# Kernel tuning notes

Hardware: AMD Instinct MI355X
Metric: run time of the kernel (lower is better)

The kernel has to match this reference:

```python
import jax, jax.numpy as jnp
import numpy as np

N, D, E = 100000, 128, 1600000
C = 1.0
MIN_NORM = 1e-15   # hgcn min_norm clamp
BALL_EPS = 4e-3    # float32 eps for proj onto Poincare ball


def artanh(x):
    # hgcn Artanh clamps input away from +-1 (use 1e-7, the fp32-representable analog of 1e-15)
    return jnp.arctanh(jnp.clip(x, -1.0 + 1e-7, 1.0 - 1e-7))


def _norm(x):
    return jnp.maximum(jnp.linalg.norm(x, axis=-1, keepdims=True), MIN_NORM)


def proj(x, c):
    norm = _norm(x)
    maxnorm = (1.0 - BALL_EPS) / jnp.sqrt(c)
    return jnp.where(norm > maxnorm, x / norm * maxnorm, x)


def expmap0(u, c):
    sc = jnp.sqrt(c)
    n = _norm(u)
    return jnp.tanh(sc * n) * u / (sc * n)


def logmap0(p, c):
    sc = jnp.sqrt(c)
    n = _norm(p)
    return artanh(sc * n) * p / (sc * n)


def mobius_add(x, y, c):
    x2 = jnp.sum(x * x, -1, keepdims=True)
    y2 = jnp.sum(y * y, -1, keepdims=True)
    xy = jnp.sum(x * y, -1, keepdims=True)
    num = (1.0 + 2.0 * c * xy + c * y2) * x + (1.0 - c * x2) * y
    den = 1.0 + 2.0 * c * xy + c * c * x2 * y2
    return num / jnp.maximum(den, MIN_NORM)


def mobius_matvec(m, x, c):
    sc = jnp.sqrt(c)
    xn = _norm(x)
    mx = x @ m.T
    mxn = _norm(mx)
    res = jnp.tanh(mxn / xn * artanh(sc * xn)) * mx / (mxn * sc)
    zero = jnp.all(mx == 0, axis=-1, keepdims=True)
    return jnp.where(zero, jnp.zeros_like(res), res)


def hgc_layer(x, edge_index, edge_weight, w, b, c_in, c_out, n):
    # HypLinear: mobius matvec + hyperbolic bias
    h = proj(mobius_matvec(w, x, c_in), c_in)
    hyp_b = proj(expmap0(b[None, :], c_in), c_in)
    h = proj(mobius_add(h, hyp_b, c_in), c_in)
    # HypAgg: aggregate in tangent space via sparse adjacency (spmm)
    xt = logmap0(h, c_in)                                   # [N, D]
    msg = xt[edge_index[1]] * edge_weight[:, None]          # [E, D]
    agg = jax.ops.segment_sum(msg, edge_index[0], num_segments=n)
    h = proj(expmap0(agg, c_in), c_in)
    # HypAct: relu in tangent space, re-map to ball at c_out
    xt = jax.nn.relu(logmap0(h, c_in))
    return proj(expmap0(xt, c_out), c_out)


def setup_inputs() -> dict:
    key = jax.random.key(0)
    ks = jax.random.split(key, 8)
    x = jax.random.normal(ks[0], (N, D), dtype=jnp.float32)
    edge_index = jax.random.randint(ks[1], (2, E), 0, N, dtype=jnp.int64 if jax.config.jax_enable_x64 else jnp.int32)
    edge_weight = jax.random.uniform(ks[2], (E,), dtype=jnp.float32)
    s = 1.0 / np.sqrt(D)
    w1 = jax.random.normal(ks[3], (D, D), dtype=jnp.float32) * s
    b1 = jax.random.normal(ks[4], (D,), dtype=jnp.float32) * s
    w2 = jax.random.normal(ks[5], (D, D), dtype=jnp.float32) * s
    b2 = jax.random.normal(ks[6], (D,), dtype=jnp.float32) * s
    return {"x": x, "edge_index": edge_index, "edge_weight": edge_weight,
            "w1": w1, "b1": b1, "w2": w2, "b2": b2}


def reference(x, edge_index, edge_weight, w1, b1, w2, b2):
    c = jnp.float32(C)
    n = x.shape[0]
    # encode(): proj_tan0 is identity on the Poincare ball
    xh = proj(expmap0(x, c), c)
    h = hgc_layer(xh, edge_index, edge_weight, w1, b1, c, c, n)
    h = hgc_layer(h, edge_index, edge_weight, w2, b2, c, c, n)
    return h
```

## Files before the change

kernel.cpp:

```cpp
#include <hip/hip_runtime.h>
#include <math.h>
#include <stdint.h>

#define D 128
#define MAXNORM (1.0f - 4e-3f)
#define ART_CLAMP 0.9999999f
#define BKT_BITS 7
#define BKT_NODES 128
#define BKT_CAP 4096
#define NB_ROWN 1024

typedef __attribute__((ext_vector_type(8))) short short8;
typedef __attribute__((ext_vector_type(4))) float float4v;
typedef __attribute__((ext_vector_type(4))) int intv4;

__device__ __forceinline__ float waveAllReduce(float v) {
#pragma unroll
    for (int off = 32; off; off >>= 1) v += __shfl_xor(v, off, 64);
    return v;
}

__device__ __forceinline__ float reduce16(float v) {
    v += __shfl_xor(v, 8, 64);
    v += __shfl_xor(v, 4, 64);
// ... 197 lines not shown
    int wv = tid >> 6;
    int tx = lane & 15;
    int q = lane >> 4;
    int sw = tx & 7;
    int row0 = rowOff + gbid * 64;

    short8 wh[2][4], wl[2][4];
#pragma unroll
    for (int c = 0; c < 2; c++) {
        int wrow = 16 * (2 * wv + c) + tx;
        const uint16_t* ph = Whi + (size_t)wrow * D + q * 8;
        const uint16_t* pl = Wlo + (size_t)wrow * D + q * 8;
#pragma unroll
        for (int t = 0; t < 4; t++) {
            wh[c][t] = *(const short8*)(ph + t * 32);
            wl[c][t] = *(const short8*)(pl + t * 32);
        }
    }

    float hbf[8];
#pragma unroll
    for (int c = 0; c < 8; c++) hbf[c] = HB[16 * c + tx];
    float hbsq = 0.f;
#pragma unroll
    for (int c = 0; c < 8; c++) hbsq += hbf[c] * hbf[c];
    float hb2 = reduce16(hbsq);

    auto loadA = [&](int tau, float4& v0, float4& v1) {
        int gr = row0 + tau * 16 + tx;
        if (gr >= n) gr = n - 1;
        const float4* ap = (const float4*)(A + (size_t)gr * D + wv * 32 + q * 8);
        v0 = ap[0];
        v1 = ap[1];
    };
    auto splitStore = [&](int b, float4 v0, float4 v1) {
        float v[8] = {v0.x, v0.y, v0.z, v0.w, v1.x, v1.y, v1.z, v1.w};
        short8 hi, lo;
        split8(v, &hi, &lo);
        int pch = (4 * wv + q) ^ sw;
        L->Ah[b][tx][pch] = hi;
        L->Al[b][tx][pch] = lo;
    };

    float4 pa0, pa1;
    loadA(0, pa0, pa1);
    splitStore(0, pa0, pa1);
    loadA(1, pa0, pa1);
    __syncthreads();

#pragma unroll
    for (int tau = 0; tau < 4; tau++) {
        int b = tau & 1;
        float4v acc[2];
        acc[0] = (float4v){0.f, 0.f, 0.f, 0.f};
        acc[1] = (float4v){0.f, 0.f, 0.f, 0.f};
#pragma unroll
        for (int t = 0; t < 4; t++) {
            int pch = (4 * t + q) ^ sw;
            short8 ahi = L->Ah[b][tx][pch];
            short8 alo = L->Al[b][tx][pch];
#pragma unroll
            for (int c = 0; c < 2; c++) {
                acc[c] = __builtin_amdgcn_mfma_f32_16x16x32_bf16(ahi, wh[c][t], acc[c], 0, 0, 0);
                acc[c] = __builtin_amdgcn_mfma_f32_16x16x32_bf16(ahi, wl[c][t], acc[c], 0, 0, 0);
                acc[c] = __builtin_amdgcn_mfma_f32_16x16x32_bf16(alo, wh[c][t], acc[c], 0, 0, 0);
            }
        }

#pragma unroll
        for (int c = 0; c < 2; c++) {
            int col = 16 * (2 * wv + c) + tx;
#pragma unroll
            for (int p = 0; p < 4; p++) {
                int lr = 4 * q + p;
                L->Cs[lr * CS_STRIDE + ((col + 4 * lr) & 127)] = acc[c][p];
            }
        }

        if (tau < 3) {
            splitStore(b ^ 1, pa0, pa1);
            if (tau < 2) loadA(tau + 2, pa0, pa1);
        }
        __syncthreads();

        int lr = 4 * wv + q;
        int row = row0 + tau * 16 + lr;
        if (row < n) {
            float y[8];
#pragma unroll
            for (int c = 0; c < 8; c++)
                y[c] = L->Cs[lr * CS_STRIDE + ((16 * c + tx + 4 * lr) & 127)];

            float s = 0.f;
#pragma unroll
            for (int c = 0; c < 8; c++) s += y[c] * y[c];
            float yn2 = reduce16(s);
            float sc, xns;
            if (ENCODE) {
                float nn = fmaxf(XN[row], 1e-15f);
                float t = fast_tanh(nn);
                sc = t * rcpf(nn);
                float pn = fmaxf(t, 1e-15f);
                if (pn > MAXNORM) { sc *= MAXNORM * rcpf(pn); pn = MAXNORM; }
                xns = pn;
            } else {
                sc = 1.0f;
                xns = fmaxf(XN[row], 1e-15f);
            }
            float mxn2 = sc * sc * yn2;
            float mxn = fmaxf(fsqrtf(mxn2), 1e-15f);
            float arg = (mxn * rcpf(xns)) * fast_atanh(fminf(xns, ART_CLAMP));
            float t = fast_tanh(arg);
            float s2 = (mxn2 == 0.0f) ? 0.0f : (sc * t * rcpf(mxn));
            float h[8];
#pragma unroll
            for (int c = 0; c < 8; c++) h[c] = y[c] * s2;
            float rn = fmaxf(t, 1e-15f);
            float hn = rn;
            if (rn > MAXNORM) {
                float f = MAXNORM * rcpf(rn);
#pragma unroll
                for (int c = 0; c < 8; c++) h[c] *= f;
                hn = MAXNORM;
            }
            float x2 = hn * hn;
            float d0 = 0.f;
#pragma unroll
            for (int c = 0; c < 8; c++) d0 += h[c] * hbf[c];
            float xy = reduce16(d0);
            float k1 = 1.0f + 2.0f * xy + hb2;
            float k2 = 1.0f - x2;
            float den = fmaxf(1.0f + 2.0f * xy + x2 * hb2, 1e-15f);
            float rden = rcpf(den);
            float av[8];
            float s3 = 0.f;
#pragma unroll
            for (int c = 0; c < 8; c++) {
                av[c] = (k1 * h[c] + k2 * hbf[c]) * rden;
                s3 += av[c] * av[c];
            }
            float an = fmaxf(fsqrtf(reduce16(s3)), 1e-15f);
            float fproj = 1.0f;
            if (an > MAXNORM) { fproj = MAXNORM * rcpf(an); an = MAXNORM; }
            float lm = fproj * fast_atanh(fminf(an, ART_CLAMP)) * rcpf(an);
            uint16_t* o = XT + (size_t)row * D + tx;
#pragma unroll
            for (int c = 0; c < 8; c++) o[16 * c] = f2bf(av[c] * lm);
        }
        __syncthreads();
    }
}


__global__ __launch_bounds__(256) void fusedPre(
    const float* __restrict__ X, float* __restrict__ XN, int n,
    const int* __restrict__ DST, int* __restrict__ bcnt, int* __restrict__ Hcnt,
    int E, int B, int gH,
    const float* __restrict__ W1, const float* __restrict__ W2,
    uint16_t* __restrict__ Whi1, uint16_t* __restrict__ Wlo1,
    uint16_t* __restrict__ Whi2, uint16_t* __restrict__ Wlo2,
    const float* __restrict__ B1, const float* __restrict__ B2,
    float* __restrict__ HBOUT) {
    __shared__ int cnt[1024];
    int bid = blockIdx.x, tid = threadIdx.x;
    if (bid < NB_ROWN) {
        rowNorms_body(bid, tid, X, XN, n);
    } else if (bid < NB_ROWN + gH) {
        histo_body(bid - NB_ROWN, tid, DST, bcnt, Hcnt, E, B, cnt);
    } else if (bid < NB_ROWN + gH + 64) {
        prepW_body(bid - NB_ROWN - gH, tid, W1, W2, Whi1, Wlo1, Whi2, Wlo2);
    } else {
        bias_body(bid - NB_ROWN - gH - 64, tid, B1, B2, HBOUT);
    }
}

__global__ __launch_bounds__(1024) void bucketScan(const int* __restrict__ bcnt,
                                                   int* __restrict__ boff,
                                                   int* __restrict__ rp_last,
                                                   int B, int E) {
    __shared__ int sd[1024];
    int tid = threadIdx.x;
    int v = (tid < B) ? bcnt[tid] : 0;
    sd[tid] = v;
    __syncthreads();
    for (int off = 1; off < 1024; off <<= 1) {
        int t = (tid >= off) ? sd[tid - off] : 0;
        __syncthreads();
        sd[tid] += t;
        __syncthreads();
    }
    int ex = sd[tid] - v;
    if (tid < B) boff[tid] = ex;
    if (tid == 0) { boff[B] = E; *rp_last = E; }
}

__global__ __launch_bounds__(256) void scanA(const int* __restrict__ boff,
                                             const int* __restrict__ Hcnt,
                                             int* __restrict__ Hbase, int B, int gH) {
    __shared__ int sd[256];
    int b = blockIdx.x;
    int k = threadIdx.x;
    int base0 = boff[b];
    int carry = 0;
    for (int k0 = 0; k0 < gH; k0 += 256) {
        int kk = k0 + k;
        int v = (kk < gH) ? Hcnt[(size_t)kk * B + b] : 0;
        sd[k] = v;
        __syncthreads();
        for (int off = 1; off < 256; off <<= 1) {
            int t = (k >= off) ? sd[k - off] : 0;
            __syncthreads();
            sd[k] += t;
            __syncthreads();
        }
        if (kk < gH) Hbase[(size_t)kk * B + b] = base0 + carry + sd[k] - v;
        carry += sd[255];
        __syncthreads();
    }
}

__global__ __launch_bounds__(256, 3) void fusedBinGemm(
    const int* __restrict__ DST, const int* __restrict__ SRC,
    const float* __restrict__ EW, const int* __restrict__ Hbase,
    int2* __restrict__ binned, int E, int B, int gBin,
    const float* __restrict__ A, const uint16_t* __restrict__ Whi,
    const uint16_t* __restrict__ Wlo, const float* __restrict__ XN,
    const float* __restrict__ HB, uint16_t* __restrict__ XT, int n) {
    __shared__ LdsBG u;
    int bid = blockIdx.x, tid = threadIdx.x;
    if (bid < gBin)
        binEdges_body(bid, tid, DST, SRC, EW, Hbase, binned, E, B, u.b.cnt, u.b.base);
    else
        gemm_body<true>(bid - gBin, 0, tid, A, Whi, Wlo, XN, HB, XT, n, &u.g);
}

__global__ __launch_bounds__(256, 3) void fusedSortGemm(
    int2* __restrict__ binned, const int* __restrict__ boff,
    int* __restrict__ rp, int n, int gSort,
    const float* __restrict__ A, const uint16_t* __restrict__ Whi,
    const uint16_t* __restrict__ Wlo, const float* __restrict__ XN,
    const float* __restrict__ HB, uint16_t* __restrict__ XT, int rowOff) {
    __shared__ LdsSG u;
    int bid = blockIdx.x, tid = threadIdx.x;
    if (bid < gSort)
        sort_body(bid, tid, binned, boff, rp, n, u.s.cnt, u.s.cur, u.s.buf);
    else
        gemm_body<true>(bid - gSort, rowOff, tid, A, Whi, Wlo, XN, HB, XT, n, &u.g);
}

template <bool ENCODE>
__global__ __launch_bounds__(256, 3) void gemmM(const float* __restrict__ A,
                                                const uint16_t* __restrict__ Whi,
                                                const uint16_t* __restrict__ Wlo,
                                                const float* __restrict__ XN,
                                                const float* __restrict__ HB,
                                                uint16_t* __restrict__ XT, int n) {
    __shared__ GemmLds L;
    gemm_body<ENCODE>(blockIdx.x, 0, threadIdx.x, A, Whi, Wlo, XN, HB, XT, n, &L);
}


template <bool STORE_HN>
__global__ __launch_bounds__(256) void aggC(const uint16_t* __restrict__ XT,
                                            const int* __restrict__ rp,
                                            const int2* __restrict__ sorted,
                                            float* __restrict__ OUT,
                                            float* __restrict__ HN, int n) {
    int tid = threadIdx.x;
    int lane = tid & 63;
    int q = lane >> 4;
    int tx = lane & 15;
    int wv = (blockIdx.x * 256 + tid) >> 6;
    int g = wv * 4 + q;
    bool valid = (g < n);
    int gc = valid ? g : (n - 1);
    uint32_t beg = (uint32_t)rp[gc];
    uint32_t end = valid ? (uint32_t)rp[gc + 1] : beg;
    uint32_t deg = end - beg;

    int m = (int)deg;
    m = max(m, __shfl_xor(m, 16, 64));
    m = max(m, __shfl_xor(m, 32, 64));
    int ms = __builtin_amdgcn_readfirstlane(m);

    const char* sbase = (const char*)sorted;
    const char* xbase = (const char*)XT;
    uint32_t txoff = (uint32_t)tx * 16u;
    uint32_t jb = beg * 8u;
    uint32_t jendb = end * 8u;
    uint32_t jlastb = (jendb > 0u) ? (jendb - 8u) : 0u;

    float a[8];
#pragma unroll
    for (int c = 0; c < 8; c++) a[c] = 0.f;

    int2 e0 = *(const int2*)(sbase + min(jb, jlastb));
    int2 e1 = *(const int2*)(sbase + min(jb + 8u, jlastb));
    int2 e2 = *(const int2*)(sbase + min(jb + 16u, jlastb));
    int2 e3 = *(const int2*)(sbase + min(jb + 24u, jlastb));
    for (int i = 0; i < ms; i += 4) {
        int2 f0 = *(const int2*)(sbase + min(jb + 32u, jlastb));
        int2 f1 = *(const int2*)(sbase + min(jb + 40u, jlastb));
        int2 f2 = *(const int2*)(sbase + min(jb + 48u, jlastb));
        int2 f3 = *(const int2*)(sbase + min(jb + 56u, jlastb));
        intv4 u0 = *(const intv4*)(xbase + ((((uint32_t)e0.x) << 8) + txoff));
        intv4 u1 = *(const intv4*)(xbase + ((((uint32_t)e1.x) << 8) + txoff));
        intv4 u2 = *(const intv4*)(xbase + ((((uint32_t)e2.x) << 8) + txoff));
        intv4 u3 = *(const intv4*)(xbase + ((((uint32_t)e3.x) << 8) + txoff));
        float w0 = (jb < jendb) ? __int_as_float(e0.y) : 0.f;
        float w1 = (jb + 8u < jendb) ? __int_as_float(e1.y) : 0.f;
        float w2 = (jb + 16u < jendb) ? __int_as_float(e2.y) : 0.f;
        float w3 = (jb + 24u < jendb) ? __int_as_float(e3.y) : 0.f;
#pragma unroll
        for (int k = 0; k < 4; k++) {
            a[2 * k]     = fmaf(__uint_as_float(((uint32_t)u0[k]) << 16), w0, a[2 * k]);
            a[2 * k + 1] = fmaf(__uint_as_float(((uint32_t)u0[k]) & 0xFFFF0000u), w0, a[2 * k + 1]);
        }
#pragma unroll
        for (int k = 0; k < 4; k++) {
            a[2 * k]     = fmaf(__uint_as_float(((uint32_t)u1[k]) << 16), w1, a[2 * k]);
            a[2 * k + 1] = fmaf(__uint_as_float(((uint32_t)u1[k]) & 0xFFFF0000u), w1, a[2 * k + 1]);
        }
#pragma unroll
        for (int k = 0; k < 4; k++) {
            a[2 * k]     = fmaf(__uint_as_float(((uint32_t)u2[k]) << 16), w2, a[2 * k]);
            a[2 * k + 1] = fmaf(__uint_as_float(((uint32_t)u2[k]) & 0xFFFF0000u), w2, a[2 * k + 1]);
        }
#pragma unroll
        for (int k = 0; k < 4; k++) {
            a[2 * k]     = fmaf(__uint_as_float(((uint32_t)u3[k]) << 16), w3, a[2 * k]);
            a[2 * k + 1] = fmaf(__uint_as_float(((uint32_t)u3[k]) & 0xFFFF0000u), w3, a[2 * k + 1]);
        }
        jb += 32u;
        e0 = f0; e1 = f1; e2 = f2; e3 = f3;
    }

    float ss = 0.f;
#pragma unroll
    for (int c = 0; c < 8; c++) ss += a[c] * a[c];
    float nn = fmaxf(fsqrtf(reduce16(ss)), 1e-15f);
    float t = fast_tanh(nn);
    float sc = t * rcpf(nn);
    float pn = fmaxf(t, 1e-15f);
    if (pn > MAXNORM) { sc *= MAXNORM * rcpf(pn); pn = MAXNORM; }
    float lm = fast_atanh(fminf(pn, ART_CLAMP)) * rcpf(pn);
    float r[8];
    float ss2 = 0.f;
#pragma unroll
    for (int c = 0; c < 8; c++) {
        r[c] = fmaxf(lm * sc * a[c], 0.f);
        ss2 += r[c] * r[c];
    }
    float rn = fmaxf(fsqrtf(reduce16(ss2)), 1e-15f);
    float t2 = fast_tanh(rn);
    float sc2 = t2 * rcpf(rn);
    float on = fmaxf(t2, 1e-15f);
    if (on > MAXNORM) { sc2 *= MAXNORM * rcpf(on); on = MAXNORM; }
    if (valid) {
        float4* o = (float4*)(OUT + (size_t)g * D + tx * 8);
        o[0] = make_float4(r[0] * sc2, r[1] * sc2, r[2] * sc2, r[3] * sc2);
        o[1] = make_float4(r[4] * sc2, r[5] * sc2, r[6] * sc2, r[7] * sc2);
        if (STORE_HN && tx == 0) HN[g] = on;
    }
}


extern "C" void kernel_launch(void* const* d_in, const int* in_sizes, int n_in,
                              void* d_out, int out_size, void* d_ws, size_t ws_size,
                              hipStream_t stream) {
    const float* x  = (const float*)d_in[0];
    const int*   ei = (const int*)d_in[1];
    const float* ew = (const float*)d_in[2];
    const float* w1 = (const float*)d_in[3];
    const float* b1 = (const float*)d_in[4];
    const float* w2 = (const float*)d_in[5];
    const float* b2 = (const float*)d_in[6];
    int n = in_sizes[0] / D;
    int E = in_sizes[2];
    int B = (n + BKT_NODES - 1) >> BKT_BITS;

    uint16_t* xtb = (uint16_t*)d_ws;
    int*   bcnt = (int*)(xtb + (size_t)n * D);
    int*   boff = bcnt + 1024;
    int*   gcur = boff + 1025;
    int*   rp   = gcur + 1024;
    float* xn   = (float*)(rp + n + 1);
    uint16_t* whi1 = (uint16_t*)(((uintptr_t)(xn + n) + 15) & ~(uintptr_t)15);
    uint16_t* wlo1 = whi1 + 128 * 128;
    uint16_t* whi2 = wlo1 + 128 * 128;
    uint16_t* wlo2 = whi2 + 128 * 128;
    float* hb = (float*)(wlo2 + 128 * 128);
    uintptr_t p = (uintptr_t)(hb + 2 * D);
    int2* binned = (int2*)((p + 15) & ~(uintptr_t)15);
    float* Hd = (float*)d_out;

    const int* dst = ei;
    const int* src = ei + E;

    const int gE8 = (E + 8191) / 8192;
    int* Hcnt  = (int*)(binned + E);
    int* Hbase = Hcnt + (size_t)gE8 * B;

    const int gG = (n + 63) / 64;
    const int GA = min(256, gG);
    const int GB = gG - GA;
    const int gAgg = (n + 15) / 16;

    hipMemsetAsync(bcnt, 0, 1024 * sizeof(int), stream);

    fusedPre<<<NB_ROWN + gE8 + 64 + 2, 256, 0, stream>>>(
        x, xn, n, dst, bcnt, Hcnt, E, B, gE8,
        w1, w2, whi1, wlo1, whi2, wlo2, b1, b2, hb);

    bucketScan<<<1, 1024, 0, stream>>>(bcnt, boff, rp + n, B, E);

    scanA<<<B, 256, 0, stream>>>(boff, Hcnt, Hbase, B, gE8);

    fusedBinGemm<<<gE8 + GA, 256, 0, stream>>>(
        dst, src, ew, Hbase, binned, E, B, gE8,
        x, whi1, wlo1, xn, hb, xtb, n);

    fusedSortGemm<<<B + GB, 256, 0, stream>>>(
        binned, boff, rp, n, B,
        x, whi1, wlo1, xn, hb, xtb, GA * 64);

    aggC<true><<<gAgg, 256, 0, stream>>>(xtb, rp, binned, Hd, xn, n);
    gemmM<false><<<gG, 256, 0, stream>>>(Hd, whi2, wlo2, xn, hb + D, xtb, n);
    aggC<false><<<gAgg, 256, 0, stream>>>(xtb, rp, binned, (float*)d_out, nullptr, n);
}
```

Before: 377.0 us.

## Fuse layer-1 aggregation with layer-2 hyperbolic linear into one kernel

```diff
diff --git a/kernel.cpp b/kernel.cpp
--- a/kernel.cpp
+++ b/kernel.cpp
@@ -586,6 +586,221 @@
 }
 
 
+__global__ __launch_bounds__(256, 4) void aggGemm(
+    const uint16_t* __restrict__ XTin, const int* __restrict__ rp,
+    const int2* __restrict__ sorted,
+    const uint16_t* __restrict__ Whi, const uint16_t* __restrict__ Wlo,
+    const float* __restrict__ HB, uint16_t* __restrict__ XTout, int n) {
+    __shared__ short8 Fh[16][16];
+    __shared__ short8 Fl[16][16];
+    __shared__ float Cs[16 * CS_STRIDE];
+    __shared__ float hnr[16];
+    int tid = threadIdx.x;
+    int lane = tid & 63;
+    int wv = tid >> 6;
+    int tx = lane & 15;
+    int q = lane >> 4;
+    int sw = tx & 7;
+    int row0 = blockIdx.x * 16;
+
+    int lr = wv * 4 + q;
+    int g = row0 + lr;
+    bool valid = (g < n);
+    int gc = valid ? g : (n - 1);
+    uint32_t beg = (uint32_t)rp[gc];
+    uint32_t end = valid ? (uint32_t)rp[gc + 1] : beg;
+    uint32_t deg = end - beg;
+    int m = (int)deg;
+    m = max(m, __shfl_xor(m, 16, 64));
+    m = max(m, __shfl_xor(m, 32, 64));
+    int ms = __builtin_amdgcn_readfirstlane(m);
+
+    const char* sbase = (const char*)sorted;
+    const char* xbase = (const char*)XTin;
+    uint32_t txoff = (uint32_t)tx * 16u;
+    uint32_t jb = beg * 8u;
+    uint32_t jendb = end * 8u;
+    uint32_t jlastb = (jendb > 0u) ? (jendb - 8u) : 0u;
+
+    float a[8];
+#pragma unroll
+    for (int c = 0; c < 8; c++) a[c] = 0.f;
+
+    int2 e0 = *(const int2*)(sbase + min(jb, jlastb));
+    int2 e1 = *(const int2*)(sbase + min(jb + 8u, jlastb));
+    int2 e2 = *(const int2*)(sbase + min(jb + 16u, jlastb));
+    int2 e3 = *(const int2*)(sbase + min(jb + 24u, jlastb));
+    for (int i = 0; i < ms; i += 4) {
+        int2 f0 = *(const int2*)(sbase + min(jb + 32u, jlastb));
+        int2 f1 = *(const int2*)(sbase + min(jb + 40u, jlastb));
+        int2 f2 = *(const int2*)(sbase + min(jb + 48u, jlastb));
+        int2 f3 = *(const int2*)(sbase + min(jb + 56u, jlastb));
+        intv4 u0 = *(const intv4*)(xbase + ((((uint32_t)e0.x) << 8) + txoff));
+        intv4 u1 = *(const intv4*)(xbase + ((((uint32_t)e1.x) << 8) + txoff));
+        intv4 u2 = *(const intv4*)(xbase + ((((uint32_t)e2.x) << 8) + txoff));
+        intv4 u3 = *(const intv4*)(xbase + ((((uint32_t)e3.x) << 8) + txoff));
+        float w0 = (jb < jendb) ? __int_as_float(e0.y) : 0.f;
+        float w1 = (jb + 8u < jendb) ? __int_as_float(e1.y) : 0.f;
+        float w2 = (jb + 16u < jendb) ? __int_as_float(e2.y) : 0.f;
+        float w3 = (jb + 24u < jendb) ? __int_as_float(e3.y) : 0.f;
+#pragma unroll
+        for (int k = 0; k < 4; k++) {
+            a[2 * k]     = fmaf(__uint_as_float(((uint32_t)u0[k]) << 16), w0, a[2 * k]);
+            a[2 * k + 1] = fmaf(__uint_as_float(((uint32_t)u0[k]) & 0xFFFF0000u), w0, a[2 * k + 1]);
+        }
+#pragma unroll
+        for (int k = 0; k < 4; k++) {
+            a[2 * k]     = fmaf(__uint_as_float(((uint32_t)u1[k]) << 16), w1, a[2 * k]);
+            a[2 * k + 1] = fmaf(__uint_as_float(((uint32_t)u1[k]) & 0xFFFF0000u), w1, a[2 * k + 1]);
+        }
+#pragma unroll
+        for (int k = 0; k < 4; k++) {
+            a[2 * k]     = fmaf(__uint_as_float(((uint32_t)u2[k]) << 16), w2, a[2 * k]);
+            a[2 * k + 1] = fmaf(__uint_as_float(((uint32_t)u2[k]) & 0xFFFF0000u), w2, a[2 * k + 1]);
+        }
+#pragma unroll
+        for (int k = 0; k < 4; k++) {
+            a[2 * k]     = fmaf(__uint_as_float(((uint32_t)u3[k]) << 16), w3, a[2 * k]);
+            a[2 * k + 1] = fmaf(__uint_as_float(((uint32_t)u3[k]) & 0xFFFF0000u), w3, a[2 * k + 1]);
+        }
+        jb += 32u;
+        e0 = f0; e1 = f1; e2 = f2; e3 = f3;
+    }
+
+    {
+        float ss = 0.f;
+#pragma unroll
+        for (int c = 0; c < 8; c++) ss += a[c] * a[c];
+        float nn = fmaxf(fsqrtf(reduce16(ss)), 1e-15f);
+        float t = fast_tanh(nn);
+        float sc = t * rcpf(nn);
+        float pn = fmaxf(t, 1e-15f);
+        if (pn > MAXNORM) { sc *= MAXNORM * rcpf(pn); pn = MAXNORM; }
+        float lm = fast_atanh(fminf(pn, ART_CLAMP)) * rcpf(pn);
+        float r[8];
+        float ss2 = 0.f;
+#pragma unroll
+        for (int c = 0; c < 8; c++) {
+            r[c] = fmaxf(lm * sc * a[c], 0.f);
+            ss2 += r[c] * r[c];
+        }
+        float rn = fmaxf(fsqrtf(reduce16(ss2)), 1e-15f);
+        float t2 = fast_tanh(rn);
+        float sc2 = t2 * rcpf(rn);
+        float on = fmaxf(t2, 1e-15f);
+        if (on > MAXNORM) { sc2 *= MAXNORM * rcpf(on); on = MAXNORM; }
+        float hv[8];
+#pragma unroll
+        for (int c = 0; c < 8; c++) hv[c] = r[c] * sc2;
+        short8 fhi, flo;
+        split8(hv, &fhi, &flo);
+        Fh[lr][tx ^ (lr & 7)] = fhi;
+        Fl[lr][tx ^ (lr & 7)] = flo;
+        if (tx == 0) hnr[lr] = on;
+    }
+    __syncthreads();
+
+    short8 wh[2][4], wl[2][4];
+#pragma unroll
+    for (int c = 0; c < 2; c++) {
+        int wrow = 16 * (2 * wv + c) + tx;
+        const uint16_t* ph = Whi + (size_t)wrow * D + q * 8;
+        const uint16_t* pl = Wlo + (size_t)wrow * D + q * 8;
+#pragma unroll
+        for (int t = 0; t < 4; t++) {
+            wh[c][t] = *(const short8*)(ph + t * 32);
+            wl[c][t] = *(const short8*)(pl + t * 32);
+        }
+    }
+    float hbf[8];
+#pragma unroll
+    for (int c = 0; c < 8; c++) hbf[c] = HB[16 * c + tx];
+    float hbsq = 0.f;
+#pragma unroll
+    for (int c = 0; c < 8; c++) hbsq += hbf[c] * hbf[c];
+    float hb2 = reduce16(hbsq);
+
+    float4v acc[2];
+    acc[0] = (float4v){0.f, 0.f, 0.f, 0.f};
+    acc[1] = (float4v){0.f, 0.f, 0.f, 0.f};
+#pragma unroll
+    for (int t = 0; t < 4; t++) {
+        int pch = (4 * t + q) ^ sw;
+        short8 ahi = Fh[tx][pch];
+        short8 alo = Fl[tx][pch];
+#pragma unroll
+        for (int c = 0; c < 2; c++) {
+            acc[c] = __builtin_amdgcn_mfma_f32_16x16x32_bf16(ahi, wh[c][t], acc[c], 0, 0, 0);
+            acc[c] = __builtin_amdgcn_mfma_f32_16x16x32_bf16(ahi, wl[c][t], acc[c], 0, 0, 0);
+            acc[c] = __builtin_amdgcn_mfma_f32_16x16x32_bf16(alo, wh[c][t], acc[c], 0, 0, 0);
+        }
+    }
+#pragma unroll
+    for (int c = 0; c < 2; c++) {
+        int col = 16 * (2 * wv + c) + tx;
+#pragma unroll
+        for (int p = 0; p < 4; p++) {
+            int lr2 = 4 * q + p;
+            Cs[lr2 * CS_STRIDE + ((col + 4 * lr2) & 127)] = acc[c][p];
+        }
+    }
+    __syncthreads();
+
+    int er = 4 * wv + q;
+    int row = row0 + er;
+    if (row < n) {
+        float y[8];
+#pragma unroll
+        for (int c = 0; c < 8; c++)
+            y[c] = Cs[er * CS_STRIDE + ((16 * c + tx + 4 * er) & 127)];
+        float s = 0.f;
+#pragma unroll
+        for (int c = 0; c < 8; c++) s += y[c] * y[c];
+        float yn2 = reduce16(s);
+        float xns = fmaxf(hnr[er], 1e-15f);
+        float mxn2 = yn2;
+        float mxn = fmaxf(fsqrtf(mxn2), 1e-15f);
+        float arg = (mxn * rcpf(xns)) * fast_atanh(fminf(xns, ART_CLAMP));
+        float tg = fast_tanh(arg);
+        float s2 = (mxn2 == 0.0f) ? 0.0f : (tg * rcpf(mxn));
+        float h[8];
+#pragma unroll
+        for (int c = 0; c < 8; c++) h[c] = y[c] * s2;
+        float rn2 = fmaxf(tg, 1e-15f);
+        float hn = rn2;
+        if (rn2 > MAXNORM) {
+            float f = MAXNORM * rcpf(rn2);
+#pragma unroll
+            for (int c = 0; c < 8; c++) h[c] *= f;
+            hn = MAXNORM;
+        }
+        float x2 = hn * hn;
+        float d0 = 0.f;
+#pragma unroll
+        for (int c = 0; c < 8; c++) d0 += h[c] * hbf[c];
+        float xy = reduce16(d0);
+        float k1 = 1.0f + 2.0f * xy + hb2;
+        float k2 = 1.0f - x2;
+        float den = fmaxf(1.0f + 2.0f * xy + x2 * hb2, 1e-15f);
+        float rden = rcpf(den);
+        float av[8];
+        float s3 = 0.f;
+#pragma unroll
+        for (int c = 0; c < 8; c++) {
+            av[c] = (k1 * h[c] + k2 * hbf[c]) * rden;
+            s3 += av[c] * av[c];
+        }
+        float an = fmaxf(fsqrtf(reduce16(s3)), 1e-15f);
+        float fproj = 1.0f;
+        if (an > MAXNORM) { fproj = MAXNORM * rcpf(an); an = MAXNORM; }
+        float lm2 = fproj * fast_atanh(fminf(an, ART_CLAMP)) * rcpf(an);
+        uint16_t* o = XTout + (size_t)row * D + tx;
+#pragma unroll
+        for (int c = 0; c < 8; c++) o[16 * c] = f2bf(av[c] * lm2);
+    }
+}
+
+
 extern "C" void kernel_launch(void* const* d_in, const int* in_sizes, int n_in,
                               void* d_out, int out_size, void* d_ws, size_t ws_size,
                               hipStream_t stream) {
@@ -621,6 +836,9 @@
     const int gE8 = (E + 8191) / 8192;
     int* Hcnt  = (int*)(binned + E);
     int* Hbase = Hcnt + (size_t)gE8 * B;
+    uint16_t* xtb2 = (uint16_t*)(Hbase + (size_t)gE8 * B);
+    size_t need = (size_t)((char*)(xtb2 + (size_t)n * D) - (char*)d_ws);
+    bool fused = (ws_size >= need);
 
     const int gG = (n + 63) / 64;
     const int GA = min(256, gG);
@@ -645,7 +863,13 @@
         binned, boff, rp, n, B,
         x, whi1, wlo1, xn, hb, xtb, GA * 64);
 
-    aggC<true><<<gAgg, 256, 0, stream>>>(xtb, rp, binned, Hd, xn, n);
-    gemmM<false><<<gG, 256, 0, stream>>>(Hd, whi2, wlo2, xn, hb + D, xtb, n);
-    aggC<false><<<gAgg, 256, 0, stream>>>(xtb, rp, binned, (float*)d_out, nullptr, n);
-}
+    if (fused) {
+        aggGemm<<<gAgg, 256, 0, stream>>>(xtb, rp, binned, whi2, wlo2,
+                                          hb + D, xtb2, n);
+        aggC<false><<<gAgg, 256, 0, stream>>>(xtb2, rp, binned, (float*)d_out, nullptr, n);
+    } else {
+        aggC<true><<<gAgg, 256, 0, stream>>>(xtb, rp, binned, Hd, xn, n);
+        gemmM<false><<<gG, 256, 0, stream>>>(Hd, whi2, wlo2, xn, hb + D, xtb, n);
+        aggC<false><<<gAgg, 256, 0, stream>>>(xtb, rp, binned, (float*)d_out, nullptr, n);
+    }
+}
```

Result: slower. 399.6 us (+6.0%).

## Pipeline layer-1 aggregation with layer-2 GEMM in row chunks

Applied to the files above, without the earlier changes.

```diff
diff --git a/kernel.cpp b/kernel.cpp
--- a/kernel.cpp
+++ b/kernel.cpp
@@ -373,6 +373,110 @@
 }
 
 
+template <bool STORE_HN>
+__device__ __forceinline__ void agg_body(int gbid, int nodeOff, int tid,
+                                         const uint16_t* __restrict__ XT,
+                                         const int* __restrict__ rp,
+                                         const int2* __restrict__ sorted,
+                                         float* __restrict__ OUT,
+                                         float* __restrict__ HN, int n) {
+    int lane = tid & 63;
+    int q = lane >> 4;
+    int tx = lane & 15;
+    int g = nodeOff + gbid * 16 + (tid >> 6) * 4 + q;
+    bool valid = (g < n);
+    int gc = valid ? g : (n - 1);
+    uint32_t beg = (uint32_t)rp[gc];
+    uint32_t end = valid ? (uint32_t)rp[gc + 1] : beg;
+    uint32_t deg = end - beg;
+
+    int m = (int)deg;
+    m = max(m, __shfl_xor(m, 16, 64));
+    m = max(m, __shfl_xor(m, 32, 64));
+    int ms = __builtin_amdgcn_readfirstlane(m);
+
+    const char* sbase = (const char*)sorted;
+    const char* xbase = (const char*)XT;
+    uint32_t txoff = (uint32_t)tx * 16u;
+    uint32_t jb = beg * 8u;
+    uint32_t jendb = end * 8u;
+    uint32_t jlastb = (jendb > 0u) ? (jendb - 8u) : 0u;
+
+    float a[8];
+#pragma unroll
+    for (int c = 0; c < 8; c++) a[c] = 0.f;
+
+    int2 e0 = *(const int2*)(sbase + min(jb, jlastb));
+    int2 e1 = *(const int2*)(sbase + min(jb + 8u, jlastb));
+    int2 e2 = *(const int2*)(sbase + min(jb + 16u, jlastb));
+    int2 e3 = *(const int2*)(sbase + min(jb + 24u, jlastb));
+    for (int i = 0; i < ms; i += 4) {
+        int2 f0 = *(const int2*)(sbase + min(jb + 32u, jlastb));
+        int2 f1 = *(const int2*)(sbase + min(jb + 40u, jlastb));
+        int2 f2 = *(const int2*)(sbase + min(jb + 48u, jlastb));
+        int2 f3 = *(const int2*)(sbase + min(jb + 56u, jlastb));
+        intv4 u0 = *(const intv4*)(xbase + ((((uint32_t)e0.x) << 8) + txoff));
+        intv4 u1 = *(const intv4*)(xbase + ((((uint32_t)e1.x) << 8) + txoff));
+        intv4 u2 = *(const intv4*)(xbase + ((((uint32_t)e2.x) << 8) + txoff));
+        intv4 u3 = *(const intv4*)(xbase + ((((uint32_t)e3.x) << 8) + txoff));
+        float w0 = (jb < jendb) ? __int_as_float(e0.y) : 0.f;
+        float w1 = (jb + 8u < jendb) ? __int_as_float(e1.y) : 0.f;
+        float w2 = (jb + 16u < jendb) ? __int_as_float(e2.y) : 0.f;
+        float w3 = (jb + 24u < jendb) ? __int_as_float(e3.y) : 0.f;
+#pragma unroll
+        for (int k = 0; k < 4; k++) {
+            a[2 * k]     = fmaf(__uint_as_float(((uint32_t)u0[k]) << 16), w0, a[2 * k]);
+            a[2 * k + 1] = fmaf(__uint_as_float(((uint32_t)u0[k]) & 0xFFFF0000u), w0, a[2 * k + 1]);
+        }
+#pragma unroll
+        for (int k = 0; k < 4; k++) {
+            a[2 * k]     = fmaf(__uint_as_float(((uint32_t)u1[k]) << 16), w1, a[2 * k]);
+            a[2 * k + 1] = fmaf(__uint_as_float(((uint32_t)u1[k]) & 0xFFFF0000u), w1, a[2 * k + 1]);
+        }
+#pragma unroll
+        for (int k = 0; k < 4; k++) {
+            a[2 * k]     = fmaf(__uint_as_float(((uint32_t)u2[k]) << 16), w2, a[2 * k]);
+            a[2 * k + 1] = fmaf(__uint_as_float(((uint32_t)u2[k]) & 0xFFFF0000u), w2, a[2 * k + 1]);
+        }
+#pragma unroll
+        for (int k = 0; k < 4; k++) {
+            a[2 * k]     = fmaf(__uint_as_float(((uint32_t)u3[k]) << 16), w3, a[2 * k]);
+            a[2 * k + 1] = fmaf(__uint_as_float(((uint32_t)u3[k]) & 0xFFFF0000u), w3, a[2 * k + 1]);
+        }
+        jb += 32u;
+        e0 = f0; e1 = f1; e2 = f2; e3 = f3;
+    }
+
+    float ss = 0.f;
+#pragma unroll
+    for (int c = 0; c < 8; c++) ss += a[c] * a[c];
+    float nn = fmaxf(fsqrtf(reduce16(ss)), 1e-15f);
+    float t = fast_tanh(nn);
+    float sc = t * rcpf(nn);
+    float pn = fmaxf(t, 1e-15f);
+    if (pn > MAXNORM) { sc *= MAXNORM * rcpf(pn); pn = MAXNORM; }
+    float lm = fast_atanh(fminf(pn, ART_CLAMP)) * rcpf(pn);
+    float r[8];
+    float ss2 = 0.f;
+#pragma unroll
+    for (int c = 0; c < 8; c++) {
+        r[c] = fmaxf(lm * sc * a[c], 0.f);
+        ss2 += r[c] * r[c];
+    }
+    float rn = fmaxf(fsqrtf(reduce16(ss2)), 1e-15f);
+    float t2 = fast_tanh(rn);
+    float sc2 = t2 * rcpf(rn);
+    float on = fmaxf(t2, 1e-15f);
+    if (on > MAXNORM) { sc2 *= MAXNORM * rcpf(on); on = MAXNORM; }
+    if (valid) {
+        float4* o = (float4*)(OUT + (size_t)g * D + tx * 8);
+        o[0] = make_float4(r[0] * sc2, r[1] * sc2, r[2] * sc2, r[3] * sc2);
+        o[1] = make_float4(r[4] * sc2, r[5] * sc2, r[6] * sc2, r[7] * sc2);
+        if (STORE_HN && tx == 0) HN[g] = on;
+    }
+}
+
+
 __global__ __launch_bounds__(256) void fusedPre(
     const float* __restrict__ X, float* __restrict__ XN, int n,
     const int* __restrict__ DST, int* __restrict__ bcnt, int* __restrict__ Hcnt,
@@ -475,114 +579,35 @@
                                                 const uint16_t* __restrict__ Wlo,
                                                 const float* __restrict__ XN,
                                                 const float* __restrict__ HB,
-                                                uint16_t* __restrict__ XT, int n) {
+                                                uint16_t* __restrict__ XT, int n,
+                                                int rowOff) {
     __shared__ GemmLds L;
-    gemm_body<ENCODE>(blockIdx.x, 0, threadIdx.x, A, Whi, Wlo, XN, HB, XT, n, &L);
-}
-
+    gemm_body<ENCODE>(blockIdx.x, rowOff, threadIdx.x, A, Whi, Wlo, XN, HB, XT, n, &L);
+}
 
 template <bool STORE_HN>
 __global__ __launch_bounds__(256) void aggC(const uint16_t* __restrict__ XT,
                                             const int* __restrict__ rp,
                                             const int2* __restrict__ sorted,
                                             float* __restrict__ OUT,
-                                            float* __restrict__ HN, int n) {
-    int tid = threadIdx.x;
-    int lane = tid & 63;
-    int q = lane >> 4;
-    int tx = lane & 15;
-    int wv = (blockIdx.x * 256 + tid) >> 6;
-    int g = wv * 4 + q;
-    bool valid = (g < n);
-    int gc = valid ? g : (n - 1);
-    uint32_t beg = (uint32_t)rp[gc];
-    uint32_t end = valid ? (uint32_t)rp[gc + 1] : beg;
-    uint32_t deg = end - beg;
-
-    int m = (int)deg;
-    m = max(m, __shfl_xor(m, 16, 64));
-    m = max(m, __shfl_xor(m, 32, 64));
-    int ms = __builtin_amdgcn_readfirstlane(m);
-
-    const char* sbase = (const char*)sorted;
-    const char* xbase = (const char*)XT;
-    uint32_t txoff = (uint32_t)tx * 16u;
-    uint32_t jb = beg * 8u;
-    uint32_t jendb = end * 8u;
-    uint32_t jlastb = (jendb > 0u) ? (jendb - 8u) : 0u;
-
-    float a[8];
-#pragma unroll
-    for (int c = 0; c < 8; c++) a[c] = 0.f;
-
-    int2 e0 = *(const int2*)(sbase + min(jb, jlastb));
-    int2 e1 = *(const int2*)(sbase + min(jb + 8u, jlastb));
-    int2 e2 = *(const int2*)(sbase + min(jb + 16u, jlastb));
-    int2 e3 = *(const int2*)(sbase + min(jb + 24u, jlastb));
-    for (int i = 0; i < ms; i += 4) {
-        int2 f0 = *(const int2*)(sbase + min(jb + 32u, jlastb));
-        int2 f1 = *(const int2*)(sbase + min(jb + 40u, jlastb));
-        int2 f2 = *(const int2*)(sbase + min(jb + 48u, jlastb));
-        int2 f3 = *(const int2*)(sbase + min(jb + 56u, jlastb));
-        intv4 u0 = *(const intv4*)(xbase + ((((uint32_t)e0.x) << 8) + txoff));
-        intv4 u1 = *(const intv4*)(xbase + ((((uint32_t)e1.x) << 8) + txoff));
-        intv4 u2 = *(const intv4*)(xbase + ((((uint32_t)e2.x) << 8) + txoff));
-        intv4 u3 = *(const intv4*)(xbase + ((((uint32_t)e3.x) << 8) + txoff));
-        float w0 = (jb < jendb) ? __int_as_float(e0.y) : 0.f;
-        float w1 = (jb + 8u < jendb) ? __int_as_float(e1.y) : 0.f;
-        float w2 = (jb + 16u < jendb) ? __int_as_float(e2.y) : 0.f;
-        float w3 = (jb + 24u < jendb) ? __int_as_float(e3.y) : 0.f;
-#pragma unroll
-        for (int k = 0; k < 4; k++) {
-            a[2 * k]     = fmaf(__uint_as_float(((uint32_t)u0[k]) << 16), w0, a[2 * k]);
-            a[2 * k + 1] = fmaf(__uint_as_float(((uint32_t)u0[k]) & 0xFFFF0000u), w0, a[2 * k + 1]);
-        }
-#pragma unroll
-        for (int k = 0; k < 4; k++) {
-            a[2 * k]     = fmaf(__uint_as_float(((uint32_t)u1[k]) << 16), w1, a[2 * k]);
-            a[2 * k + 1] = fmaf(__uint_as_float(((uint32_t)u1[k]) & 0xFFFF0000u), w1, a[2 * k + 1]);
-        }
-#pragma unroll
-        for (int k = 0; k < 4; k++) {
-            a[2 * k]     = fmaf(__uint_as_float(((uint32_t)u2[k]) << 16), w2, a[2 * k]);
-            a[2 * k + 1] = fmaf(__uint_as_float(((uint32_t)u2[k]) & 0xFFFF0000u), w2, a[2 * k + 1]);
-        }
-#pragma unroll
-        for (int k = 0; k < 4; k++) {
-            a[2 * k]     = fmaf(__uint_as_float(((uint32_t)u3[k]) << 16), w3, a[2 * k]);
-            a[2 * k + 1] = fmaf(__uint_as_float(((uint32_t)u3[k]) & 0xFFFF0000u), w3, a[2 * k + 1]);
-        }
-        jb += 32u;
-        e0 = f0; e1 = f1; e2 = f2; e3 = f3;
-    }
-
-    float ss = 0.f;
-#pragma unroll
-    for (int c = 0; c < 8; c++) ss += a[c] * a[c];
-    float nn = fmaxf(fsqrtf(reduce16(ss)), 1e-15f);
-    float t = fast_tanh(nn);
-    float sc = t * rcpf(nn);
-    float pn = fmaxf(t, 1e-15f);
-    if (pn > MAXNORM) { sc *= MAXNORM * rcpf(pn); pn = MAXNORM; }
-    float lm = fast_atanh(fminf(pn, ART_CLAMP)) * rcpf(pn);
-    float r[8];
-    float ss2 = 0.f;
-#pragma unroll
-    for (int c = 0; c < 8; c++) {
-        r[c] = fmaxf(lm * sc * a[c], 0.f);
-        ss2 += r[c] * r[c];
-    }
-    float rn = fmaxf(fsqrtf(reduce16(ss2)), 1e-15f);
-    float t2 = fast_tanh(rn);
-    float sc2 = t2 * rcpf(rn);
-    float on = fmaxf(t2, 1e-15f);
-    if (on > MAXNORM) { sc2 *= MAXNORM * rcpf(on); on = MAXNORM; }
-    if (valid) {
-        float4* o = (float4*)(OUT + (size_t)g * D + tx * 8);
-        o[0] = make_float4(r[0] * sc2, r[1] * sc2, r[2] * sc2, r[3] * sc2);
-        o[1] = make_float4(r[4] * sc2, r[5] * sc2, r[6] * sc2, r[7] * sc2);
-        if (STORE_HN && tx == 0) HN[g] = on;
-    }
+                                            float* __restrict__ HN, int n,
+                                            int nodeOff) {
+    agg_body<STORE_HN>(blockIdx.x, nodeOff, threadIdx.x, XT, rp, sorted, OUT, HN, n);
+}
+
+__global__ __launch_bounds__(256, 4) void fusedAggGemm(
+    const uint16_t* __restrict__ XT1, const int* __restrict__ rp,
+    const int2* __restrict__ sorted, float* __restrict__ Hd,
+    float* __restrict__ HN, int nAgg, int nodeOff, int n,
+    const uint16_t* __restrict__ Whi, const uint16_t* __restrict__ Wlo,
+    const float* __restrict__ XN, const float* __restrict__ HB,
+    uint16_t* __restrict__ XTout, int gemmRowOff) {
+    __shared__ GemmLds L;
+    int bid = blockIdx.x, tid = threadIdx.x;
+    if (bid < nAgg)
+        agg_body<true>(bid, nodeOff, tid, XT1, rp, sorted, Hd, HN, n);
+    else
+        gemm_body<false>(bid - nAgg, gemmRowOff, tid, Hd, Whi, Wlo, XN, HB, XTout, n, &L);
 }
 
 
@@ -621,11 +646,14 @@
     const int gE8 = (E + 8191) / 8192;
     int* Hcnt  = (int*)(binned + E);
     int* Hbase = Hcnt + (size_t)gE8 * B;
+    uint16_t* xtb2 = (uint16_t*)(Hbase + (size_t)gE8 * B);
+    size_t need = (size_t)((char*)(xtb2 + (size_t)n * D) - (char*)d_ws);
 
     const int gG = (n + 63) / 64;
     const int GA = min(256, gG);
     const int GB = gG - GA;
     const int gAgg = (n + 15) / 16;
+    bool pipelined = (ws_size >= need) && (gG >= 8);
 
     hipMemsetAsync(bcnt, 0, 1024 * sizeof(int), stream);
 
@@ -645,7 +673,26 @@
         binned, boff, rp, n, B,
         x, whi1, wlo1, xn, hb, xtb, GA * 64);
 
-    aggC<true><<<gAgg, 256, 0, stream>>>(xtb, rp, binned, Hd, xn, n);
-    gemmM<false><<<gG, 256, 0, stream>>>(Hd, whi2, wlo2, xn, hb + D, xtb, n);
-    aggC<false><<<gAgg, 256, 0, stream>>>(xtb, rp, binned, (float*)d_out, nullptr, n);
-}
+    if (pipelined) {
+        const int gG4 = gG / 4;
+        const int R1 = gG4 * 64, R2 = 2 * gG4 * 64, R3 = 3 * gG4 * 64;
+        const int a0 = R1 / 16, a1 = (R2 - R1) / 16, a2 = (R3 - R2) / 16;
+        const int a3 = (n - R3 + 15) / 16;
+        aggC<true><<<a0, 256, 0, stream>>>(xtb, rp, binned, Hd, xn, n, 0);
+        fusedAggGemm<<<a1 + gG4, 256, 0, stream>>>(
+            xtb, rp, binned, Hd, xn, a1, R1, n, whi2, wlo2, xn, hb + D, xtb2, 0);
+        fusedAggGemm<<<a2 + gG4, 256, 0, stream>>>(
+            xtb, rp, binned, Hd, xn, a2, R2, n, whi2, wlo2, xn, hb + D, xtb2, R1);
+        fusedAggGemm<<<a3 + gG4, 256, 0, stream>>>(
+            xtb, rp, binned, Hd, xn, a3, R3, n, whi2, wlo2, xn, hb + D, xtb2, R2);
+        gemmM<false><<<gG - 3 * gG4, 256, 0, stream>>>(Hd, whi2, wlo2, xn,
+                                                       hb + D, xtb2, n, R3);
+        aggC<false><<<gAgg, 256, 0, stream>>>(xtb2, rp, binned, (float*)d_out,
+                                              nullptr, n, 0);
+    } else {
+        aggC<true><<<gAgg, 256, 0, stream>>>(xtb, rp, binned, Hd, xn, n, 0);
+        gemmM<false><<<gG, 256, 0, stream>>>(Hd, whi2, wlo2, xn, hb + D, xtb, n, 0);
+        aggC<false><<<gAgg, 256, 0, stream>>>(xtb, rp, binned, (float*)d_out,
+                                              nullptr, n, 0);
+    }
+}
```

New measurement: 432.1 us. 14.6% more time.

## Sort aggregation rows by degree to balance wave divergence in SpMM

Applied to the files above, without the earlier changes.

```diff
diff --git a/kernel.cpp b/kernel.cpp
--- a/kernel.cpp
+++ b/kernel.cpp
@@ -373,6 +373,111 @@
 }
 
 
+template <bool STORE_HN>
+__device__ __forceinline__ void agg_body(int gbid, int tid,
+                                         const uint16_t* __restrict__ XT,
+                                         const int* __restrict__ rp,
+                                         const int2* __restrict__ sorted,
+                                         const int* __restrict__ perm,
+                                         float* __restrict__ OUT,
+                                         float* __restrict__ HN, int n) {
+    int lane = tid & 63;
+    int q = lane >> 4;
+    int tx = lane & 15;
+    int idx = gbid * 16 + (tid >> 6) * 4 + q;
+    bool valid = (idx < n);
+    int g = valid ? (perm ? perm[idx] : idx) : (n - 1);
+    uint32_t beg = (uint32_t)rp[g];
+    uint32_t end = valid ? (uint32_t)rp[g + 1] : beg;
+    uint32_t deg = end - beg;
+
+    int m = (int)deg;
+    m = max(m, __shfl_xor(m, 16, 64));
+    m = max(m, __shfl_xor(m, 32, 64));
+    int ms = __builtin_amdgcn_readfirstlane(m);
+
+    const char* sbase = (const char*)sorted;
+    const char* xbase = (const char*)XT;
+    uint32_t txoff = (uint32_t)tx * 16u;
+    uint32_t jb = beg * 8u;
+    uint32_t jendb = end * 8u;
+    uint32_t jlastb = (jendb > 0u) ? (jendb - 8u) : 0u;
+
+    float a[8];
+#pragma unroll
+    for (int c = 0; c < 8; c++) a[c] = 0.f;
+
+    int2 e0 = *(const int2*)(sbase + min(jb, jlastb));
+    int2 e1 = *(const int2*)(sbase + min(jb + 8u, jlastb));
+    int2 e2 = *(const int2*)(sbase + min(jb + 16u, jlastb));
+    int2 e3 = *(const int2*)(sbase + min(jb + 24u, jlastb));
+    for (int i = 0; i < ms; i += 4) {
+        int2 f0 = *(const int2*)(sbase + min(jb + 32u, jlastb));
+        int2 f1 = *(const int2*)(sbase + min(jb + 40u, jlastb));
+        int2 f2 = *(const int2*)(sbase + min(jb + 48u, jlastb));
+        int2 f3 = *(const int2*)(sbase + min(jb + 56u, jlastb));
+        intv4 u0 = *(const intv4*)(xbase + ((((uint32_t)e0.x) << 8) + txoff));
+        intv4 u1 = *(const intv4*)(xbase + ((((uint32_t)e1.x) << 8) + txoff));
+        intv4 u2 = *(const intv4*)(xbase + ((((uint32_t)e2.x) << 8) + txoff));
+        intv4 u3 = *(const intv4*)(xbase + ((((uint32_t)e3.x) << 8) + txoff));
+        float w0 = (jb < jendb) ? __int_as_float(e0.y) : 0.f;
+        float w1 = (jb + 8u < jendb) ? __int_as_float(e1.y) : 0.f;
+        float w2 = (jb + 16u < jendb) ? __int_as_float(e2.y) : 0.f;
+        float w3 = (jb + 24u < jendb) ? __int_as_float(e3.y) : 0.f;
+#pragma unroll
+        for (int k = 0; k < 4; k++) {
+            a[2 * k]     = fmaf(__uint_as_float(((uint32_t)u0[k]) << 16), w0, a[2 * k]);
+            a[2 * k + 1] = fmaf(__uint_as_float(((uint32_t)u0[k]) & 0xFFFF0000u), w0, a[2 * k + 1]);
+        }
+#pragma unroll
+        for (int k = 0; k < 4; k++) {
+            a[2 * k]     = fmaf(__uint_as_float(((uint32_t)u1[k]) << 16), w1, a[2 * k]);
+            a[2 * k + 1] = fmaf(__uint_as_float(((uint32_t)u1[k]) & 0xFFFF0000u), w1, a[2 * k + 1]);
+        }
+#pragma unroll
+        for (int k = 0; k < 4; k++) {
+            a[2 * k]     = fmaf(__uint_as_float(((uint32_t)u2[k]) << 16), w2, a[2 * k]);
+            a[2 * k + 1] = fmaf(__uint_as_float(((uint32_t)u2[k]) & 0xFFFF0000u), w2, a[2 * k + 1]);
+        }
+#pragma unroll
+        for (int k = 0; k < 4; k++) {
+            a[2 * k]     = fmaf(__uint_as_float(((uint32_t)u3[k]) << 16), w3, a[2 * k]);
+            a[2 * k + 1] = fmaf(__uint_as_float(((uint32_t)u3[k]) & 0xFFFF0000u), w3, a[2 * k + 1]);
+        }
+        jb += 32u;
+        e0 = f0; e1 = f1; e2 = f2; e3 = f3;
+    }
+
+    float ss = 0.f;
+#pragma unroll
+    for (int c = 0; c < 8; c++) ss += a[c] * a[c];
+    float nn = fmaxf(fsqrtf(reduce16(ss)), 1e-15f);
+    float t = fast_tanh(nn);
+    float sc = t * rcpf(nn);
+    float pn = fmaxf(t, 1e-15f);
+    if (pn > MAXNORM) { sc *= MAXNORM * rcpf(pn); pn = MAXNORM; }
+    float lm = fast_atanh(fminf(pn, ART_CLAMP)) * rcpf(pn);
+    float r[8];
+    float ss2 = 0.f;
+#pragma unroll
+    for (int c = 0; c < 8; c++) {
+        r[c] = fmaxf(lm * sc * a[c], 0.f);
+        ss2 += r[c] * r[c];
+    }
+    float rn = fmaxf(fsqrtf(reduce16(ss2)), 1e-15f);
+    float t2 = fast_tanh(rn);
+    float sc2 = t2 * rcpf(rn);
+    float on = fmaxf(t2, 1e-15f);
+    if (on > MAXNORM) { sc2 *= MAXNORM * rcpf(on); on = MAXNORM; }
+    if (valid) {
+        float4* o = (float4*)(OUT + (size_t)g * D + tx * 8);
+        o[0] = make_float4(r[0] * sc2, r[1] * sc2, r[2] * sc2, r[3] * sc2);
+        o[1] = make_float4(r[4] * sc2, r[5] * sc2, r[6] * sc2, r[7] * sc2);
+        if (STORE_HN && tx == 0) HN[g] = on;
+    }
+}
+
+
 __global__ __launch_bounds__(256) void fusedPre(
     const float* __restrict__ X, float* __restrict__ XN, int n,
     const int* __restrict__ DST, int* __restrict__ bcnt, int* __restrict__ Hcnt,
@@ -480,109 +585,56 @@
     gemm_body<ENCODE>(blockIdx.x, 0, threadIdx.x, A, Whi, Wlo, XN, HB, XT, n, &L);
 }
 
-
 template <bool STORE_HN>
 __global__ __launch_bounds__(256) void aggC(const uint16_t* __restrict__ XT,
                                             const int* __restrict__ rp,
                                             const int2* __restrict__ sorted,
+                                            const int* __restrict__ perm,
                                             float* __restrict__ OUT,
                                             float* __restrict__ HN, int n) {
+    agg_body<STORE_HN>(blockIdx.x, threadIdx.x, XT, rp, sorted, perm, OUT, HN, n);
+}
+
+
+__global__ __launch_bounds__(256) void degHisto(const int* __restrict__ rp,
+                                                int* __restrict__ dhist, int n) {
+    __shared__ int h[256];
     int tid = threadIdx.x;
-    int lane = tid & 63;
-    int q = lane >> 4;
-    int tx = lane & 15;
-    int wv = (blockIdx.x * 256 + tid) >> 6;
-    int g = wv * 4 + q;
-    bool valid = (g < n);
-    int gc = valid ? g : (n - 1);
-    uint32_t beg = (uint32_t)rp[gc];
-    uint32_t end = valid ? (uint32_t)rp[gc + 1] : beg;
-    uint32_t deg = end - beg;
-
-    int m = (int)deg;
-    m = max(m, __shfl_xor(m, 16, 64));
-    m = max(m, __shfl_xor(m, 32, 64));
-    int ms = __builtin_amdgcn_readfirstlane(m);
-
-    const char* sbase = (const char*)sorted;
-    const char* xbase = (const char*)XT;
-    uint32_t txoff = (uint32_t)tx * 16u;
-    uint32_t jb = beg * 8u;
-    uint32_t jendb = end * 8u;
-    uint32_t jlastb = (jendb > 0u) ? (jendb - 8u) : 0u;
-
-    float a[8];
-#pragma unroll
-    for (int c = 0; c < 8; c++) a[c] = 0.f;
-
-    int2 e0 = *(const int2*)(sbase + min(jb, jlastb));
-    int2 e1 = *(const int2*)(sbase + min(jb + 8u, jlastb));
-    int2 e2 = *(const int2*)(sbase + min(jb + 16u, jlastb));
-    int2 e3 = *(const int2*)(sbase + min(jb + 24u, jlastb));
-    for (int i = 0; i < ms; i += 4) {
-        int2 f0 = *(const int2*)(sbase + min(jb + 32u, jlastb));
-        int2 f1 = *(const int2*)(sbase + min(jb + 40u, jlastb));
-        int2 f2 = *(const int2*)(sbase + min(jb + 48u, jlastb));
-        int2 f3 = *(const int2*)(sbase + min(jb + 56u, jlastb));
-        intv4 u0 = *(const intv4*)(xbase + ((((uint32_t)e0.x) << 8) + txoff));
-        intv4 u1 = *(const intv4*)(xbase + ((((uint32_t)e1.x) << 8) + txoff));
-        intv4 u2 = *(const intv4*)(xbase + ((((uint32_t)e2.x) << 8) + txoff));
-        intv4 u3 = *(const intv4*)(xbase + ((((uint32_t)e3.x) << 8) + txoff));
-        float w0 = (jb < jendb) ? __int_as_float(e0.y) : 0.f;
-        float w1 = (jb + 8u < jendb) ? __int_as_float(e1.y) : 0.f;
-        float w2 = (jb + 16u < jendb) ? __int_as_float(e2.y) : 0.f;
-        float w3 = (jb + 24u < jendb) ? __int_as_float(e3.y) : 0.f;
-#pragma unroll
-        for (int k = 0; k < 4; k++) {
-            a[2 * k]     = fmaf(__uint_as_float(((uint32_t)u0[k]) << 16), w0, a[2 * k]);
-            a[2 * k + 1] = fmaf(__uint_as_float(((uint32_t)u0[k]) & 0xFFFF0000u), w0, a[2 * k + 1]);
-        }
-#pragma unroll
-        for (int k = 0; k < 4; k++) {
-            a[2 * k]     = fmaf(__uint_as_float(((uint32_t)u1[k]) << 16), w1, a[2 * k]);
-            a[2 * k + 1] = fmaf(__uint_as_float(((uint32_t)u1[k]) & 0xFFFF0000u), w1, a[2 * k + 1]);
-        }
-#pragma unroll
-        for (int k = 0; k < 4; k++) {
-            a[2 * k]     = fmaf(__uint_as_float(((uint32_t)u2[k]) << 16), w2, a[2 * k]);
-            a[2 * k + 1] = fmaf(__uint_as_float(((uint32_t)u2[k]) & 0xFFFF0000u), w2, a[2 * k + 1]);
-        }
-#pragma unroll
-        for (int k = 0; k < 4; k++) {
-            a[2 * k]     = fmaf(__uint_as_float(((uint32_t)u3[k]) << 16), w3, a[2 * k]);
-            a[2 * k + 1] = fmaf(__uint_as_float(((uint32_t)u3[k]) & 0xFFFF0000u), w3, a[2 * k + 1]);
-        }
-        jb += 32u;
-        e0 = f0; e1 = f1; e2 = f2; e3 = f3;
-    }
-
-    float ss = 0.f;
-#pragma unroll
-    for (int c = 0; c < 8; c++) ss += a[c] * a[c];
-    float nn = fmaxf(fsqrtf(reduce16(ss)), 1e-15f);
-    float t = fast_tanh(nn);
-    float sc = t * rcpf(nn);
-    float pn = fmaxf(t, 1e-15f);
-    if (pn > MAXNORM) { sc *= MAXNORM * rcpf(pn); pn = MAXNORM; }
-    float lm = fast_atanh(fminf(pn, ART_CLAMP)) * rcpf(pn);
-    float r[8];
-    float ss2 = 0.f;
-#pragma unroll
-    for (int c = 0; c < 8; c++) {
-        r[c] = fmaxf(lm * sc * a[c], 0.f);
-        ss2 += r[c] * r[c];
-    }
-    float rn = fmaxf(fsqrtf(reduce16(ss2)), 1e-15f);
-    float t2 = fast_tanh(rn);
-    float sc2 = t2 * rcpf(rn);
-    float on = fmaxf(t2, 1e-15f);
-    if (on > MAXNORM) { sc2 *= MAXNORM * rcpf(on); on = MAXNORM; }
-    if (valid) {
-        float4* o = (float4*)(OUT + (size_t)g * D + tx * 8);
-        o[0] = make_float4(r[0] * sc2, r[1] * sc2, r[2] * sc2, r[3] * sc2);
-        o[1] = make_float4(r[4] * sc2, r[5] * sc2, r[6] * sc2, r[7] * sc2);
-        if (STORE_HN && tx == 0) HN[g] = on;
-    }
+    h[tid] = 0;
+    __syncthreads();
+    int g = blockIdx.x * 256 + tid;
+    if (g < n) {
+        int d = rp[g + 1] - rp[g];
+        atomicAdd(&h[255 - min(d, 255)], 1);
+    }
+    __syncthreads();
+    if (h[tid]) atomicAdd(&dhist[tid], h[tid]);
+}
+
+__global__ __launch_bounds__(256) void degScan(const int* __restrict__ dhist,
+                                               int* __restrict__ dcur) {
+    __shared__ int sd[256];
+    int tid = threadIdx.x;
+    int v = dhist[tid];
+    sd[tid] = v;
+    __syncthreads();
+    for (int off = 1; off < 256; off <<= 1) {
+        int t = (tid >= off) ? sd[tid - off] : 0;
+        __syncthreads();
+        sd[tid] += t;
+        __syncthreads();
+    }
+    dcur[tid] = sd[tid] - v;
+}
+
+__global__ __launch_bounds__(256) void permScatter(const int* __restrict__ rp,
+                                                   int* __restrict__ dcur,
+                                                   int* __restrict__ perm, int n) {
+    int g = blockIdx.x * 256 + threadIdx.x;
+    if (g >= n) return;
+    int d = rp[g + 1] - rp[g];
+    int pos = atomicAdd(&dcur[255 - min(d, 255)], 1);
+    perm[pos] = g;
 }
 
 
@@ -621,13 +673,20 @@
     const int gE8 = (E + 8191) / 8192;
     int* Hcnt  = (int*)(binned + E);
     int* Hbase = Hcnt + (size_t)gE8 * B;
+    int* dhist = Hbase + (size_t)gE8 * B;
+    int* dcur  = dhist + 256;
+    int* perm  = dcur + 256;
+    size_t need = (size_t)((char*)(perm + n) - (char*)d_ws);
+    const int* permUse = (ws_size >= need) ? perm : nullptr;
 
     const int gG = (n + 63) / 64;
     const int GA = min(256, gG);
     const int GB = gG - GA;
     const int gAgg = (n + 15) / 16;
+    const int gN256 = (n + 255) / 256;
 
     hipMemsetAsync(bcnt, 0, 1024 * sizeof(int), stream);
+    if (permUse) hipMemsetAsync(dhist, 0, 256 * sizeof(int), stream);
 
     fusedPre<<<NB_ROWN + gE8 + 64 + 2, 256, 0, stream>>>(
         x, xn, n, dst, bcnt, Hcnt, E, B, gE8,
@@ -645,7 +704,14 @@
         binned, boff, rp, n, B,
         x, whi1, wlo1, xn, hb, xtb, GA * 64);
 
-    aggC<true><<<gAgg, 256, 0, stream>>>(xtb, rp, binned, Hd, xn, n);
+    if (permUse) {
+        degHisto<<<gN256, 256, 0, stream>>>(rp, dhist, n);
+        degScan<<<1, 256, 0, stream>>>(dhist, dcur);
+        permScatter<<<gN256, 256, 0, stream>>>(rp, dcur, perm, n);
+    }
+
+    aggC<true><<<gAgg, 256, 0, stream>>>(xtb, rp, binned, permUse, Hd, xn, n);
     gemmM<false><<<gG, 256, 0, stream>>>(Hd, whi2, wlo2, xn, hb + D, xtb, n);
-    aggC<false><<<gAgg, 256, 0, stream>>>(xtb, rp, binned, (float*)d_out, nullptr, n);
-}
+    aggC<false><<<gAgg, 256, 0, stream>>>(xtb, rp, binned, permUse,
+                                          (float*)d_out, nullptr, n);
+}
```

New measurement: 670.8 us. 1.78x slower.
